# Performance work log

Measured on AMD Instinct MI355X. Metric: run time of the kernel, lower is better.

The kernel has to match this reference:

```python
import jax, jax.numpy as jnp
import numpy as np

B, S, N, D = 32, 512, 64, 64


def setup_inputs() -> dict:
    key = jax.random.key(0)
    ks = jax.random.split(key, 6)
    return {
        "x": jax.random.normal(ks[0], (B, S, N, D), dtype=jnp.float32),
        "q_embed_weight": jax.random.normal(ks[1], (N, D), dtype=jnp.float32) * 0.02,
        "Wq_w": jax.random.normal(ks[2], (D, D), dtype=jnp.float32) * (1.0 / np.sqrt(D)),
        "Wq_b": jax.random.normal(ks[3], (D,), dtype=jnp.float32) * 0.02,
        "Wkv_w": jax.random.normal(ks[4], (2 * D, D), dtype=jnp.float32) * (1.0 / np.sqrt(D)),
        "Wkv_b": jax.random.normal(ks[5], (2 * D,), dtype=jnp.float32) * 0.02,
    }


def reference(x, q_embed_weight, Wq_w, Wq_b, Wkv_w, Wkv_b):
    d = x.shape[-1]
    # q = Wq(q_embed.weight): [n, d]
    q = q_embed_weight @ Wq_w.T + Wq_b
    # Wkv(x) -> [b, s, n, 2d]; chunk -> k is first half (v half is computed but unused, matching torch)
    kv = jnp.einsum('bsnd,ed->bsne', x, Wkv_w) + Wkv_b
    k = kv[..., :d]
    # prod: full contraction over n and d -> [b, s]
    prod = jnp.einsum('nd,bsnd->bs', q, k) / jnp.sqrt(jnp.asarray(d, x.dtype))
    attn = jax.nn.softmax(prod, axis=1)  # softmax over s
    # weighted sum over s with v = x (original overwrites v): [b, n, d]
    out = jnp.einsum('bs,bsnd->bnd', attn, x)
    return out
```

## Files before the change

### kernel.cpp

```cpp
#include <hip/hip_runtime.h>

#define B_   32
#define S_   512
#define ND_  4096
#define SCH  16
#define CH   32
#define RW   8

__global__ void qw_kernel(const float* __restrict__ qe, const float* __restrict__ Wq_w,
                          const float* __restrict__ Wq_b, const float* __restrict__ Wkv_w,
                          float* __restrict__ qw) {
    const int n = blockIdx.x;
    const int t = threadIdx.x;
    __shared__ float qrow[64];
    float acc = Wq_b[t];
    const float* qen = qe + n * 64;
    const float* wqr = Wq_w + t * 64;
#pragma unroll 8
    for (int d = 0; d < 64; ++d) acc += qen[d] * wqr[d];
    qrow[t] = acc;
    __syncthreads();
    float s = 0.f;
#pragma unroll 8
    for (int e = 0; e < 64; ++e) s += qrow[e] * Wkv_w[e * 64 + t];
    qw[n * 64 + t] = s * 0.125f;
}

__global__ __launch_bounds__(256, 2) void flash_partial(
    const float* __restrict__ x, const float* __restrict__ qw,
    float* __restrict__ po, float* __restrict__ pml) {
    const int blk = blockIdx.x;
    const int b   = blk >> 4;
    const int c   = blk & (SCH - 1);
    const int t   = threadIdx.x;
    const int w   = t >> 6;
    const int l   = t & 63;

    const float4* qw4 = (const float4*)qw;
    float4 qv[16];
#pragma unroll
    for (int j = 0; j < 16; ++j) qv[j] = qw4[j * 64 + l];

    float4 o[16];
#pragma unroll
    for (int j = 0; j < 16; ++j) o[j] = make_float4(0.f, 0.f, 0.f, 0.f);
    float m = -3.0e38f, lsum = 0.f;

    const int s0 = c * CH + w * RW;
    const float4* xb = (const float4*)(x) + (size_t)(b * S_ + s0) * 1024;

    for (int r = 0; r < RW; ++r) {
        const float4* xr = xb + (size_t)r * 1024;
        float4 cur[16];
#pragma unroll
        for (int j = 0; j < 16; ++j) cur[j] = xr[j * 64 + l];

        float pd = 0.f;
#pragma unroll
        for (int j = 0; j < 16; ++j)
            pd += cur[j].x * qv[j].x + cur[j].y * qv[j].y +
                  cur[j].z * qv[j].z + cur[j].w * qv[j].w;
#pragma unroll
        for (int off = 32; off > 0; off >>= 1)
            pd += __shfl_xor(pd, off, 64);

        const float mn = fmaxf(m, pd);
        const float sc = __expf(m - mn);
        const float wt = __expf(pd - mn);
        lsum = lsum * sc + wt;
#pragma unroll
        for (int j = 0; j < 16; ++j) {
            o[j].x = o[j].x * sc + wt * cur[j].x;
            o[j].y = o[j].y * sc + wt * cur[j].y;
            o[j].z = o[j].z * sc + wt * cur[j].z;
            o[j].w = o[j].w * sc + wt * cur[j].w;
        }
        m = mn;
    }

    __shared__ float  sml[4][2];
    __shared__ float4 obuf[1024];
    if (l == 0) { sml[w][0] = m; sml[w][1] = lsum; }
    __syncthreads();
    const float M = fmaxf(fmaxf(sml[0][0], sml[1][0]), fmaxf(sml[2][0], sml[3][0]));
    float L = 0.f;
#pragma unroll
    for (int ww = 0; ww < 4; ++ww) L += __expf(sml[ww][0] - M) * sml[ww][1];
    const float wk = __expf(sml[w][0] - M);

    if (w == 0) {
#pragma unroll
        for (int j = 0; j < 16; ++j) {
            float4 v = { wk * o[j].x, wk * o[j].y, wk * o[j].z, wk * o[j].w };
            obuf[j * 64 + l] = v;
        }
    }
    __syncthreads();
#pragma unroll
    for (int ww = 1; ww < 4; ++ww) {
        if (w == ww) {
#pragma unroll
            for (int j = 0; j < 16; ++j) {
                float4 v = obuf[j * 64 + l];
                v.x += wk * o[j].x; v.y += wk * o[j].y;
                v.z += wk * o[j].z; v.w += wk * o[j].w;
                obuf[j * 64 + l] = v;
            }
        }
        __syncthreads();
    }

    float4* pob = (float4*)(po) + (size_t)blk * 1024;
#pragma unroll
    for (int jj = 0; jj < 4; ++jj) {
        const int j = w * 4 + jj;
        pob[j * 64 + l] = obuf[j * 64 + l];
    }
    if (t == 0) { pml[blk * 2] = M; pml[blk * 2 + 1] = L; }
}

__global__ __launch_bounds__(256) void combine_kernel(
    const float* __restrict__ po, const float* __restrict__ pml,
    float* __restrict__ out) {
    const int b   = blockIdx.x >> 4;
    const int seg = blockIdx.x & 15;
    const int t   = threadIdx.x;
    const int idx = seg * 256 + t;
    __shared__ float sm[SCH], sl[SCH];
    if (t < SCH) {
        sm[t] = pml[(b * SCH + t) * 2];
        sl[t] = pml[(b * SCH + t) * 2 + 1];
    }
    __syncthreads();
    float M = -3.0e38f;
#pragma unroll
    for (int c = 0; c < SCH; ++c) M = fmaxf(M, sm[c]);
    float L = 0.f, acc = 0.f;
#pragma unroll
    for (int c = 0; c < SCH; ++c) {
        const float wc = __expf(sm[c] - M);
        L += wc * sl[c];
        acc += wc * po[(size_t)(b * SCH + c) * ND_ + idx];
    }
    out[(size_t)b * ND_ + idx] = acc / L;
}

extern "C" void kernel_launch(void* const* d_in, const int* in_sizes, int n_in,
                              void* d_out, int out_size, void* d_ws, size_t ws_size,
                              hipStream_t stream) {
    const float* x     = (const float*)d_in[0];
    const float* qe    = (const float*)d_in[1];
    const float* Wq_w  = (const float*)d_in[2];
    const float* Wq_b  = (const float*)d_in[3];
    const float* Wkv_w = (const float*)d_in[4];
    float* out = (float*)d_out;

    float* qw  = (float*)d_ws;
    float* pml = qw + ND_;
    float* po  = pml + (size_t)B_ * SCH * 2;

    qw_kernel<<<dim3(64), dim3(64), 0, stream>>>(qe, Wq_w, Wq_b, Wkv_w, qw);
    flash_partial<<<dim3(B_ * SCH), dim3(256), 0, stream>>>(x, qw, po, pml);
    combine_kernel<<<dim3(B_ * 16), dim3(256), 0, stream>>>(po, pml, out);
}
```

Baseline: 57.65 us.

## Fuse combine into flash kernel with atomic work queue and last-block reduction

```diff
diff --git a/kernel.cpp b/kernel.cpp
--- a/kernel.cpp
+++ b/kernel.cpp
@@ -1,17 +1,23 @@
 #include <hip/hip_runtime.h>
 
-#define B_   32
-#define S_   512
-#define ND_  4096
-#define SCH  16
-#define CH   32
-#define RW   8
+#define B_    32
+#define S_    512
+#define ND_   4096
+#define ND4_  1024
+#define UPB   24
+#define NUNIT (B_ * UPB)
+#define GRID_ 768
+#define CTR_OFF (ND_ + NUNIT * 2)
+#define PO_OFF  (CTR_OFF + 64)
+
+typedef float f4 __attribute__((ext_vector_type(4)));
 
 __global__ void qw_kernel(const float* __restrict__ qe, const float* __restrict__ Wq_w,
                           const float* __restrict__ Wq_b, const float* __restrict__ Wkv_w,
-                          float* __restrict__ qw) {
+                          float* __restrict__ ws) {
     const int n = blockIdx.x;
     const int t = threadIdx.x;
+    if (n == 0) ((int*)(ws + CTR_OFF))[t] = 0;
     __shared__ float qrow[64];
     float acc = Wq_b[t];
     const float* qen = qe + n * 64;
@@ -23,126 +29,135 @@
     float s = 0.f;
 #pragma unroll 8
     for (int e = 0; e < 64; ++e) s += qrow[e] * Wkv_w[e * 64 + t];
-    qw[n * 64 + t] = s * 0.125f;
+    ws[n * 64 + t] = s * 0.125f;
 }
 
-__global__ __launch_bounds__(256, 2) void flash_partial(
-    const float* __restrict__ x, const float* __restrict__ qw,
-    float* __restrict__ po, float* __restrict__ pml) {
-    const int blk = blockIdx.x;
-    const int b   = blk >> 4;
-    const int c   = blk & (SCH - 1);
-    const int t   = threadIdx.x;
-    const int w   = t >> 6;
-    const int l   = t & 63;
+__global__ __launch_bounds__(256, 3) void flash_fused(
+    const float* __restrict__ x, float* __restrict__ ws, float* __restrict__ out) {
+    float* qwg   = ws;
+    float* pml   = ws + ND_;
+    int*   workq = (int*)(ws + CTR_OFF);
+    int*   cnt   = workq + 1;
+    f4*    po    = (f4*)(ws + PO_OFF);
 
-    const float4* qw4 = (const float4*)qw;
-    float4 qv[16];
+    const int t = threadIdx.x;
+    const int w = t >> 6;
+    const int l = t & 63;
+
+    __shared__ f4   qws[ND4_];
+    __shared__ f4   obuf[ND4_];
+    __shared__ float sml[4][2];
+    __shared__ int   bcast[2];
+
 #pragma unroll
-    for (int j = 0; j < 16; ++j) qv[j] = qw4[j * 64 + l];
+    for (int k = 0; k < 4; ++k) qws[t + 256 * k] = ((const f4*)qwg)[t + 256 * k];
 
-    float4 o[16];
+    for (;;) {
+        if (t == 0) bcast[0] = atomicAdd(workq, 1);
+        __syncthreads();
+        const int u = bcast[0];
+        if (u >= NUNIT) break;
+        const int b = u / UPB;
+        const int k = u - b * UPB;
+        const int rstart = (k < 16) ? 21 * k : 22 * k - 16;
+        const int rcnt   = (k < 16) ? 21 : 22;
+        const int r0 = (rcnt * w) >> 2;
+        const int r1 = (rcnt * (w + 1)) >> 2;
+
+        const f4* xb = (const f4*)x + ((size_t)(b * S_ + rstart)) * ND4_;
+
+        f4 o[16];
 #pragma unroll
-    for (int j = 0; j < 16; ++j) o[j] = make_float4(0.f, 0.f, 0.f, 0.f);
-    float m = -3.0e38f, lsum = 0.f;
+        for (int j = 0; j < 16; ++j) o[j] = (f4)(0.f);
+        float m = -3.0e38f, lsum = 0.f;
 
-    const int s0 = c * CH + w * RW;
-    const float4* xb = (const float4*)(x) + (size_t)(b * S_ + s0) * 1024;
+        for (int r = r0; r < r1; ++r) {
+            const f4* xr = xb + (size_t)r * ND4_;
+            f4 cur[16];
+#pragma unroll
+            for (int j = 0; j < 16; ++j) cur[j] = __builtin_nontemporal_load(&xr[j * 64 + l]);
 
-    for (int r = 0; r < RW; ++r) {
-        const float4* xr = xb + (size_t)r * 1024;
-        float4 cur[16];
+            int zero = 0;
+            asm volatile("" : "+v"(zero));
+            float pd = 0.f;
 #pragma unroll
-        for (int j = 0; j < 16; ++j) cur[j] = xr[j * 64 + l];
+            for (int j = 0; j < 16; ++j) {
+                f4 qv = qws[j * 64 + l + zero];
+                pd += cur[j][0] * qv[0] + cur[j][1] * qv[1] +
+                      cur[j][2] * qv[2] + cur[j][3] * qv[3];
+            }
+#pragma unroll
+            for (int off = 32; off > 0; off >>= 1) pd += __shfl_xor(pd, off, 64);
 
-        float pd = 0.f;
+            const float mn = fmaxf(m, pd);
+            const float sc = __expf(m - mn);
+            const float wt = __expf(pd - mn);
+            lsum = lsum * sc + wt;
 #pragma unroll
-        for (int j = 0; j < 16; ++j)
-            pd += cur[j].x * qv[j].x + cur[j].y * qv[j].y +
-                  cur[j].z * qv[j].z + cur[j].w * qv[j].w;
+            for (int j = 0; j < 16; ++j) o[j] = o[j] * sc + wt * cur[j];
+            m = mn;
+        }
+
+        if (l == 0) { sml[w][0] = m; sml[w][1] = lsum; }
+        __syncthreads();
+        const float M = fmaxf(fmaxf(sml[0][0], sml[1][0]), fmaxf(sml[2][0], sml[3][0]));
+        float L = 0.f;
 #pragma unroll
-        for (int off = 32; off > 0; off >>= 1)
-            pd += __shfl_xor(pd, off, 64);
+        for (int ww = 0; ww < 4; ++ww) L += __expf(sml[ww][0] - M) * sml[ww][1];
+        const float wk = __expf(sml[w][0] - M);
+        if (w == 0) {
+#pragma unroll
+            for (int j = 0; j < 16; ++j) obuf[j * 64 + l] = wk * o[j];
+        }
+        __syncthreads();
+        for (int ww = 1; ww < 4; ++ww) {
+            if (w == ww) {
+#pragma unroll
+                for (int j = 0; j < 16; ++j) obuf[j * 64 + l] += wk * o[j];
+            }
+            __syncthreads();
+        }
 
-        const float mn = fmaxf(m, pd);
-        const float sc = __expf(m - mn);
-        const float wt = __expf(pd - mn);
-        lsum = lsum * sc + wt;
+        f4* pou = po + (size_t)u * ND4_;
 #pragma unroll
-        for (int j = 0; j < 16; ++j) {
-            o[j].x = o[j].x * sc + wt * cur[j].x;
-            o[j].y = o[j].y * sc + wt * cur[j].y;
-            o[j].z = o[j].z * sc + wt * cur[j].z;
-            o[j].w = o[j].w * sc + wt * cur[j].w;
+        for (int jj = 0; jj < 4; ++jj) {
+            const int j = w * 4 + jj;
+            pou[j * 64 + l] = obuf[j * 64 + l];
         }
-        m = mn;
-    }
+        if (t == 0) { pml[u * 2] = M; pml[u * 2 + 1] = L; }
+        __syncthreads();
 
-    __shared__ float  sml[4][2];
-    __shared__ float4 obuf[1024];
-    if (l == 0) { sml[w][0] = m; sml[w][1] = lsum; }
-    __syncthreads();
-    const float M = fmaxf(fmaxf(sml[0][0], sml[1][0]), fmaxf(sml[2][0], sml[3][0]));
-    float L = 0.f;
+        if (t == 0) {
+            __threadfence();
+            const int prev = atomicAdd(&cnt[b], 1);
+            bcast[1] = (prev == UPB - 1);
+        }
+        __syncthreads();
+
+        if (bcast[1]) {
+            __threadfence();
+            float Mg = -3.0e38f;
 #pragma unroll
-    for (int ww = 0; ww < 4; ++ww) L += __expf(sml[ww][0] - M) * sml[ww][1];
-    const float wk = __expf(sml[w][0] - M);
-
-    if (w == 0) {
+            for (int cc = 0; cc < UPB; ++cc) Mg = fmaxf(Mg, pml[(b * UPB + cc) * 2]);
+            float Lg = 0.f;
+            f4 acc[4];
 #pragma unroll
-        for (int j = 0; j < 16; ++j) {
-            float4 v = { wk * o[j].x, wk * o[j].y, wk * o[j].z, wk * o[j].w };
-            obuf[j * 64 + l] = v;
+            for (int kk = 0; kk < 4; ++kk) acc[kk] = (f4)(0.f);
+            for (int cc = 0; cc < UPB; ++cc) {
+                const float wc = __expf(pml[(b * UPB + cc) * 2] - Mg);
+                Lg += wc * pml[(b * UPB + cc) * 2 + 1];
+                const f4* pc = po + (size_t)(b * UPB + cc) * ND4_;
+#pragma unroll
+                for (int kk = 0; kk < 4; ++kk) acc[kk] += wc * pc[kk * 256 + t];
+            }
+            const float inv = 1.f / Lg;
+            f4* ob = (f4*)out + (size_t)b * 256;
+#pragma unroll
+            for (int kk = 0; kk < 4; ++kk)
+                ((f4*)out)[(size_t)b * ND4_ + kk * 256 + t] = acc[kk] * inv;
+            (void)ob;
         }
     }
-    __syncthreads();
-#pragma unroll
-    for (int ww = 1; ww < 4; ++ww) {
-        if (w == ww) {
-#pragma unroll
-            for (int j = 0; j < 16; ++j) {
-                float4 v = obuf[j * 64 + l];
-                v.x += wk * o[j].x; v.y += wk * o[j].y;
-                v.z += wk * o[j].z; v.w += wk * o[j].w;
-                obuf[j * 64 + l] = v;
-            }
-        }
-        __syncthreads();
-    }
-
-    float4* pob = (float4*)(po) + (size_t)blk * 1024;
-#pragma unroll
-    for (int jj = 0; jj < 4; ++jj) {
-        const int j = w * 4 + jj;
-        pob[j * 64 + l] = obuf[j * 64 + l];
-    }
-    if (t == 0) { pml[blk * 2] = M; pml[blk * 2 + 1] = L; }
-}
-
-__global__ __launch_bounds__(256) void combine_kernel(
-    const float* __restrict__ po, const float* __restrict__ pml,
-    float* __restrict__ out) {
-    const int b   = blockIdx.x >> 4;
-    const int seg = blockIdx.x & 15;
-    const int t   = threadIdx.x;
-    const int idx = seg * 256 + t;
-    __shared__ float sm[SCH], sl[SCH];
-    if (t < SCH) {
-        sm[t] = pml[(b * SCH + t) * 2];
-        sl[t] = pml[(b * SCH + t) * 2 + 1];
-    }
-    __syncthreads();
-    float M = -3.0e38f;
-#pragma unroll
-    for (int c = 0; c < SCH; ++c) M = fmaxf(M, sm[c]);
-    float L = 0.f, acc = 0.f;
-#pragma unroll
-    for (int c = 0; c < SCH; ++c) {
-        const float wc = __expf(sm[c] - M);
-        L += wc * sl[c];
-        acc += wc * po[(size_t)(b * SCH + c) * ND_ + idx];
-    }
-    out[(size_t)b * ND_ + idx] = acc / L;
 }
 
 extern "C" void kernel_launch(void* const* d_in, const int* in_sizes, int n_in,
@@ -154,12 +169,8 @@
     const float* Wq_b  = (const float*)d_in[3];
     const float* Wkv_w = (const float*)d_in[4];
     float* out = (float*)d_out;
+    float* ws  = (float*)d_ws;
 
-    float* qw  = (float*)d_ws;
-    float* pml = qw + ND_;
-    float* po  = pml + (size_t)B_ * SCH * 2;
-
-    qw_kernel<<<dim3(64), dim3(64), 0, stream>>>(qe, Wq_w, Wq_b, Wkv_w, qw);
-    flash_partial<<<dim3(B_ * SCH), dim3(256), 0, stream>>>(x, qw, po, pml);
-    combine_kernel<<<dim3(B_ * 16), dim3(256), 0, stream>>>(po, pml, out);
+    qw_kernel<<<dim3(64), dim3(64), 0, stream>>>(qe, Wq_w, Wq_b, Wkv_w, ws);
+    flash_fused<<<dim3(GRID_), dim3(256), 0, stream>>>(x, ws, out);
 }
```

Result: slower. 130.0 us (+125.4%).

## Stage x rows through LDS with async global_load_lds prefetch

Applied to the files above, without the earlier changes.

```diff
diff --git a/kernel.cpp b/kernel.cpp
--- a/kernel.cpp
+++ b/kernel.cpp
@@ -1,11 +1,23 @@
 #include <hip/hip_runtime.h>
+#include <stdint.h>
 
-#define B_   32
-#define S_   512
-#define ND_  4096
-#define SCH  16
-#define CH   32
-#define RW   8
+#define B_    32
+#define S_    512
+#define ND_   4096
+#define ND4_  1024
+#define SCH   16
+#define CH    32
+#define RW    8
+#define NUNIT (B_ * SCH)
+
+typedef float f4 __attribute__((ext_vector_type(4)));
+
+__device__ __forceinline__ void async16(void* lds_uniform_base, const void* g_perlane) {
+    __builtin_amdgcn_global_load_lds(
+        (const __attribute__((address_space(1))) uint32_t*)(g_perlane),
+        (__attribute__((address_space(3))) uint32_t*)(lds_uniform_base),
+        16, 0, 0);
+}
 
 __global__ void qw_kernel(const float* __restrict__ qe, const float* __restrict__ Wq_w,
                           const float* __restrict__ Wq_b, const float* __restrict__ Wkv_w,
@@ -36,30 +48,43 @@
     const int w   = t >> 6;
     const int l   = t & 63;
 
-    const float4* qw4 = (const float4*)qw;
-    float4 qv[16];
+    __shared__ char lds_raw[65536];
+    f4* stage = (f4*)(lds_raw + w * 16384);
+
+    const f4* qw4 = (const f4*)qw;
+    f4 qv[16];
 #pragma unroll
     for (int j = 0; j < 16; ++j) qv[j] = qw4[j * 64 + l];
 
-    float4 o[16];
+    f4 o[16];
 #pragma unroll
-    for (int j = 0; j < 16; ++j) o[j] = make_float4(0.f, 0.f, 0.f, 0.f);
+    for (int j = 0; j < 16; ++j) o[j] = (f4)(0.f);
     float m = -3.0e38f, lsum = 0.f;
 
     const int s0 = c * CH + w * RW;
-    const float4* xb = (const float4*)(x) + (size_t)(b * S_ + s0) * 1024;
+    const f4* xb = (const f4*)x + (size_t)(b * S_ + s0) * ND4_;
+
+#pragma unroll
+    for (int j = 0; j < 16; ++j) async16(stage + j * 64, xb + j * 64 + l);
+    asm volatile("s_waitcnt vmcnt(0)" ::: "memory");
 
     for (int r = 0; r < RW; ++r) {
-        const float4* xr = xb + (size_t)r * 1024;
-        float4 cur[16];
+        f4 cur[16];
 #pragma unroll
-        for (int j = 0; j < 16; ++j) cur[j] = xr[j * 64 + l];
+        for (int j = 0; j < 16; ++j) cur[j] = stage[j * 64 + l];
+        asm volatile("s_waitcnt lgkmcnt(0)" ::: "memory");
+
+        if (r + 1 < RW) {
+            const f4* xn = xb + (size_t)(r + 1) * ND4_;
+#pragma unroll
+            for (int j = 0; j < 16; ++j) async16(stage + j * 64, xn + j * 64 + l);
+        }
 
         float pd = 0.f;
 #pragma unroll
         for (int j = 0; j < 16; ++j)
-            pd += cur[j].x * qv[j].x + cur[j].y * qv[j].y +
-                  cur[j].z * qv[j].z + cur[j].w * qv[j].w;
+            pd += cur[j][0] * qv[j][0] + cur[j][1] * qv[j][1] +
+                  cur[j][2] * qv[j][2] + cur[j][3] * qv[j][3];
 #pragma unroll
         for (int off = 32; off > 0; off >>= 1)
             pd += __shfl_xor(pd, off, 64);
@@ -69,48 +94,38 @@
         const float wt = __expf(pd - mn);
         lsum = lsum * sc + wt;
 #pragma unroll
-        for (int j = 0; j < 16; ++j) {
-            o[j].x = o[j].x * sc + wt * cur[j].x;
-            o[j].y = o[j].y * sc + wt * cur[j].y;
-            o[j].z = o[j].z * sc + wt * cur[j].z;
-            o[j].w = o[j].w * sc + wt * cur[j].w;
-        }
+        for (int j = 0; j < 16; ++j) o[j] = o[j] * sc + wt * cur[j];
         m = mn;
+
+        if (r + 1 < RW) asm volatile("s_waitcnt vmcnt(0)" ::: "memory");
     }
 
-    __shared__ float  sml[4][2];
-    __shared__ float4 obuf[1024];
-    if (l == 0) { sml[w][0] = m; sml[w][1] = lsum; }
     __syncthreads();
-    const float M = fmaxf(fmaxf(sml[0][0], sml[1][0]), fmaxf(sml[2][0], sml[3][0]));
+    float* sml  = (float*)(lds_raw + 16384);
+    f4*    obuf = (f4*)lds_raw;
+    if (l == 0) { sml[w * 2] = m; sml[w * 2 + 1] = lsum; }
+    __syncthreads();
+    const float M = fmaxf(fmaxf(sml[0], sml[2]), fmaxf(sml[4], sml[6]));
     float L = 0.f;
 #pragma unroll
-    for (int ww = 0; ww < 4; ++ww) L += __expf(sml[ww][0] - M) * sml[ww][1];
-    const float wk = __expf(sml[w][0] - M);
+    for (int ww = 0; ww < 4; ++ww) L += __expf(sml[ww * 2] - M) * sml[ww * 2 + 1];
+    const float wk = __expf(sml[w * 2] - M);
 
     if (w == 0) {
 #pragma unroll
-        for (int j = 0; j < 16; ++j) {
-            float4 v = { wk * o[j].x, wk * o[j].y, wk * o[j].z, wk * o[j].w };
-            obuf[j * 64 + l] = v;
-        }
+        for (int j = 0; j < 16; ++j) obuf[j * 64 + l] = wk * o[j];
     }
     __syncthreads();
 #pragma unroll
     for (int ww = 1; ww < 4; ++ww) {
         if (w == ww) {
 #pragma unroll
-            for (int j = 0; j < 16; ++j) {
-                float4 v = obuf[j * 64 + l];
-                v.x += wk * o[j].x; v.y += wk * o[j].y;
-                v.z += wk * o[j].z; v.w += wk * o[j].w;
-                obuf[j * 64 + l] = v;
-            }
+            for (int j = 0; j < 16; ++j) obuf[j * 64 + l] += wk * o[j];
         }
         __syncthreads();
     }
 
-    float4* pob = (float4*)(po) + (size_t)blk * 1024;
+    f4* pob = (f4*)po + (size_t)blk * ND4_;
 #pragma unroll
     for (int jj = 0; jj < 4; ++jj) {
         const int j = w * 4 + jj;
@@ -157,9 +172,9 @@
 
     float* qw  = (float*)d_ws;
     float* pml = qw + ND_;
-    float* po  = pml + (size_t)B_ * SCH * 2;
+    float* po  = pml + (size_t)NUNIT * 2;
 
     qw_kernel<<<dim3(64), dim3(64), 0, stream>>>(qe, Wq_w, Wq_b, Wkv_w, qw);
-    flash_partial<<<dim3(B_ * SCH), dim3(256), 0, stream>>>(x, qw, po, pml);
+    flash_partial<<<dim3(NUNIT), dim3(256), 0, stream>>>(x, qw, po, pml);
     combine_kernel<<<dim3(B_ * 16), dim3(256), 0, stream>>>(po, pml, out);
 }
```

Result: slower. 58.96 us (+2.3%).
